# Optimization experiments

Measured on AMD Instinct MI355X. Metric: run time of the kernel, lower is better.

## Reference

```python
import jax, jax.numpy as jnp
import numpy as np


def quantize_ternary(w):
    # BitNet b1.58: scale by mean |w|, round, clamp to {-1,0,1}
    gamma = jnp.maximum(jnp.mean(jnp.abs(w)), 1e-8)
    return jnp.clip(jnp.round(w / gamma), -1.0, 1.0)


def setup_inputs() -> dict:
    key = jax.random.key(0)
    k1, k2, k3 = jax.random.split(key, 3)
    in_features, out_features = 4096, 4096
    x = jax.random.normal(k1, (4, 2048, in_features), dtype=jnp.float32)
    # kaiming_uniform-like init
    bound_w = 1.0 / np.sqrt(in_features)
    weight = jax.random.uniform(k2, (out_features, in_features), dtype=jnp.float32,
                                minval=-bound_w * np.sqrt(3.0), maxval=bound_w * np.sqrt(3.0))
    bias = jax.random.uniform(k3, (out_features,), dtype=jnp.float32,
                              minval=-bound_w, maxval=bound_w)
    return {"x": x, "weight": weight, "bias": bias}


def reference(x, weight, bias):
    qw = quantize_ternary(weight)  # [out, in], values in {-1,0,1}
    # F.linear: x @ qw.T + bias
    return jnp.einsum('bsi,oi->bso', x, qw) + bias
```

## Files before the change

### kernel.cpp

```cpp
#include <hip/hip_runtime.h>
#include <stdint.h>

#define M_DIM 8192
#define N_DIM 4096
#define K_DIM 4096
#define BM 256
#define BN 256
#define BKS 64
#define NSLAB (K_DIM / BKS)
#define SLOT_BYTES (256 * BKS)

typedef int i32x4 __attribute__((ext_vector_type(4)));

__device__ __forceinline__ void async_copy16(const void* g, void* l) {
    __builtin_amdgcn_global_load_lds(
        (const __attribute__((address_space(1))) void*)g,
        (__attribute__((address_space(3))) void*)l, 16, 0, 0);
}

__global__ __launch_bounds__(256) void abssum_partial(const float4* __restrict__ w,
                                                      double* __restrict__ partials) {
    const int lane = threadIdx.x & 63;
    const int wave = threadIdx.x >> 6;
    int base = blockIdx.x * 4096 + threadIdx.x;
    float s = 0.f;
    #pragma unroll
    for (int i = 0; i < 16; i++) {
        float4 v = w[base + i * 256];
        s += fabsf(v.x) + fabsf(v.y) + fabsf(v.z) + fabsf(v.w);
    }
    double d = (double)s;
    #pragma unroll
    for (int off = 32; off > 0; off >>= 1) d += __shfl_down(d, off, 64);
    __shared__ double wsum[4];
    if (lane == 0) wsum[wave] = d;
    __syncthreads();
    if (threadIdx.x == 0)
        partials[blockIdx.x] = (wsum[0] + wsum[1]) + (wsum[2] + wsum[3]);
}

__global__ __launch_bounds__(256) void gamma_reduce(const double* __restrict__ partials,
                                                    float* __restrict__ gamma_out) {
    const int lane = threadIdx.x & 63;
    const int wave = threadIdx.x >> 6;
    double d = partials[threadIdx.x] + partials[threadIdx.x + 256] +
               partials[threadIdx.x + 512] + partials[threadIdx.x + 768];
    #pragma unroll
    for (int off = 32; off > 0; off >>= 1) d += __shfl_down(d, off, 64);
    __shared__ double wsum[4];
    if (lane == 0) wsum[wave] = d;
    __syncthreads();
    if (threadIdx.x == 0) {
        double total = (wsum[0] + wsum[1]) + (wsum[2] + wsum[3]);
        float g = (float)(total * (1.0 / 16777216.0));
        gamma_out[0] = fmaxf(g, 1e-8f);
    }
}

__global__ __launch_bounds__(256) void wquant(const float4* __restrict__ w,
                                              char4* __restrict__ qw,
                                              const float* __restrict__ gamma_p, int n4) {
    float gamma = gamma_p[0];
    int i = blockIdx.x * blockDim.x + threadIdx.x;
    if (i >= n4) return;
    float4 v = w[i];
    char4 o;
    o.x = (signed char)fminf(fmaxf(rintf(v.x / gamma), -1.f), 1.f);
    o.y = (signed char)fminf(fmaxf(rintf(v.y / gamma), -1.f), 1.f);
    o.z = (signed char)fminf(fmaxf(rintf(v.z / gamma), -1.f), 1.f);
    o.w = (signed char)fminf(fmaxf(rintf(v.w / gamma), -1.f), 1.f);
    qw[i] = o;
}

__global__ __launch_bounds__(256) void xquant(const float4* __restrict__ x,
                                              char4* __restrict__ xq,
                                              float* __restrict__ xscale) {
    const int row = blockIdx.x;
    const int lane = threadIdx.x & 63;
    const int wave = threadIdx.x >> 6;
    const float4* xr = x + (size_t)row * (K_DIM / 4);
    float4 v[4];
    float m = 0.f;
    #pragma unroll
    for (int i = 0; i < 4; i++) {
        v[i] = xr[threadIdx.x + i * 256];
        m = fmaxf(m, fmaxf(fmaxf(fabsf(v[i].x), fabsf(v[i].y)),
                           fmaxf(fabsf(v[i].z), fabsf(v[i].w))));
    }
    #pragma unroll
    for (int off = 32; off > 0; off >>= 1) m = fmaxf(m, __shfl_down(m, off, 64));
    __shared__ float wmax[4];
    if (lane == 0) wmax[wave] = m;
    __syncthreads();
    const float mx = fmaxf(fmaxf(wmax[0], wmax[1]), fmaxf(wmax[2], wmax[3]));
    const float scale = fmaxf(mx * (1.f / 127.f), 1e-30f);
    const float inv = 1.f / scale;
    if (threadIdx.x == 0) xscale[row] = scale;
    char4* oq = xq + (size_t)row * (K_DIM / 4);
    #pragma unroll
    for (int i = 0; i < 4; i++) {
        char4 o;
        o.x = (signed char)fminf(fmaxf(rintf(v[i].x * inv), -127.f), 127.f);
        o.y = (signed char)fminf(fmaxf(rintf(v[i].y * inv), -127.f), 127.f);
        o.z = (signed char)fminf(fmaxf(rintf(v[i].z * inv), -127.f), 127.f);
        o.w = (signed char)fminf(fmaxf(rintf(v[i].w * inv), -127.f), 127.f);
        oq[threadIdx.x + i * 256] = o;
    }
}

__global__ __launch_bounds__(512, 2) void gemm_kernel(
    const char* __restrict__ xq,
    const char* __restrict__ qw,
    const float* __restrict__ xscale,
    const float* __restrict__ bias,
    float* __restrict__ out)
{
    __shared__ __align__(16) char As[4][SLOT_BYTES];
    __shared__ __align__(16) char Bs[4][SLOT_BYTES];

    const int tid  = threadIdx.x;
    const int wave = tid >> 6;
    const int lane = tid & 63;
    const int wm   = (wave >> 2) * 128;
    const int wn   = (wave & 3) * 64;
    const int lm   = lane & 15;
    const int q4   = lane >> 4;

    const int bm = blockIdx.y * BM;
    const int bn = blockIdx.x * BN;

    const int rsub = lane >> 2;
    const int csw  = (lane & 3) ^ ((lane >> 3) & 3);
    const char* gA[2];
    const char* gB[2];
    int ldsOff[2];
    #pragma unroll
    for (int j = 0; j < 2; j++) {
        const int r = wave * 32 + j * 16 + rsub;
        gA[j] = xq + (size_t)(bm + r) * K_DIM + csw * 16;
        gB[j] = qw + (size_t)(bn + r) * K_DIM + csw * 16;
        ldsOff[j] = (wave * 32 + j * 16) * BKS;
    }

    i32x4 acc[8][4];
    #pragma unroll
    for (int i = 0; i < 8; i++)
        #pragma unroll
        for (int j = 0; j < 4; j++) acc[i][j] = (i32x4){0, 0, 0, 0};

    const int pc = (q4 ^ ((lm >> 1) & 3)) * 16;

    auto stage_slab = [&](int ts, int slot) {
        async_copy16(gA[0] + (size_t)ts * BKS, &As[slot][ldsOff[0]]);
        async_copy16(gB[0] + (size_t)ts * BKS, &Bs[slot][ldsOff[0]]);
        async_copy16(gA[1] + (size_t)ts * BKS, &As[slot][ldsOff[1]]);
        async_copy16(gB[1] + (size_t)ts * BKS, &Bs[slot][ldsOff[1]]);
    };

    auto compute_slab = [&](const char* Ab, const char* Bb) {
        i32x4 b[4], a[8];
        #pragma unroll
        for (int ni = 0; ni < 4; ni++)
            b[ni] = *(const i32x4*)(Bb + (wn + ni * 16 + lm) * BKS + pc);
        #pragma unroll
        for (int mi = 0; mi < 8; mi++)
            a[mi] = *(const i32x4*)(Ab + (wm + mi * 16 + lm) * BKS + pc);
        __builtin_amdgcn_s_setprio(1);
        #pragma unroll
        for (int mi = 0; mi < 8; mi++)
            #pragma unroll
            for (int ni = 0; ni < 4; ni++)
                acc[mi][ni] = __builtin_amdgcn_mfma_i32_16x16x64_i8(
                    a[mi], b[ni], acc[mi][ni], 0, 0, 0);
        __builtin_amdgcn_s_setprio(0);
    };

    #pragma unroll
    for (int s = 0; s < 3; s++) stage_slab(s, s);
    asm volatile("s_waitcnt vmcnt(8)" ::: "memory");
    __builtin_amdgcn_s_barrier();

    for (int tb = 0; tb < NSLAB - 4; tb += 4) {
        #pragma unroll
        for (int u = 0; u < 4; u++) {
            stage_slab(tb + u + 3, (u + 3) & 3);
            compute_slab(As[u], Bs[u]);
            asm volatile("s_waitcnt vmcnt(8)" ::: "memory");
            __builtin_amdgcn_s_barrier();
        }
    }

    stage_slab(63, 3);
    compute_slab(As[0], Bs[0]);
    asm volatile("s_waitcnt vmcnt(8)" ::: "memory");
    __builtin_amdgcn_s_barrier();

    compute_slab(As[1], Bs[1]);
    asm volatile("s_waitcnt vmcnt(4)" ::: "memory");
    __builtin_amdgcn_s_barrier();

    compute_slab(As[2], Bs[2]);
    asm volatile("s_waitcnt vmcnt(0)" ::: "memory");
    __builtin_amdgcn_s_barrier();

    compute_slab(As[3], Bs[3]);

    float bl[4];
    #pragma unroll
    for (int ni = 0; ni < 4; ni++) bl[ni] = bias[bn + wn + ni * 16 + lm];

    #pragma unroll
    for (int mi = 0; mi < 8; mi++) {
        #pragma unroll
        for (int r = 0; r < 4; r++) {
            const int grow = bm + wm + mi * 16 + q4 * 4 + r;
            const float sc = xscale[grow];
            float* orow = out + (size_t)grow * N_DIM + bn + wn;
            #pragma unroll
            for (int ni = 0; ni < 4; ni++)
                orow[ni * 16 + lm] = sc * (float)acc[mi][ni][r] + bl[ni];
        }
    }
}

extern "C" void kernel_launch(void* const* d_in, const int* in_sizes, int n_in,
                              void* d_out, int out_size, void* d_ws, size_t ws_size,
                              hipStream_t stream) {
    const float* x    = (const float*)d_in[0];
    const float* w    = (const float*)d_in[1];
    const float* bias = (const float*)d_in[2];
    float* out = (float*)d_out;

    char* ws = (char*)d_ws;
    char*   xq       = ws;
    char*   qw       = ws + (size_t)M_DIM * K_DIM;
    float*  xscale   = (float*)(qw + (size_t)N_DIM * K_DIM);
    double* partials = (double*)(xscale + M_DIM);
    float*  gamma_p  = (float*)(partials + 1024);

    const int wn4 = (N_DIM * K_DIM) / 4;

    abssum_partial<<<1024, 256, 0, stream>>>((const float4*)w, partials);
    gamma_reduce<<<1, 256, 0, stream>>>(partials, gamma_p);
    wquant<<<(wn4 + 255) / 256, 256, 0, stream>>>((const float4*)w, (char4*)qw, gamma_p, wn4);
    xquant<<<M_DIM, 256, 0, stream>>>((const float4*)x, (char4*)xq, xscale);

    dim3 grid(N_DIM / BN, M_DIM / BM);
    gemm_kernel<<<grid, 512, 0, stream>>>(xq, qw, xscale, bias, out);
}
```

Before: 413.6 us.

## Fuse quantization prep kernels and shrink GEMM tile to 256x128 with triple buffering

The weight abs-sum and the activation quantization now run in one launch. The gamma reduction is folded into the weight-quantization kernel, which recomputes gamma in every block. Together this cuts four prep launches down to two. The GEMM block goes from 512 threads with a 256x256 tile and 4-slot LDS ring to 256 threads with a 256x128 tile and a 3-slot ring, which lowers LDS use and doubles the number of blocks. The trade-off is more redundant A loads from global memory per output and a shallower prefetch depth.

```diff
diff --git a/kernel.cpp b/kernel.cpp
--- a/kernel.cpp
+++ b/kernel.cpp
@@ -5,10 +5,11 @@
 #define N_DIM 4096
 #define K_DIM 4096
 #define BM 256
-#define BN 256
+#define BN 128
 #define BKS 64
 #define NSLAB (K_DIM / BKS)
-#define SLOT_BYTES (256 * BKS)
+#define A_SLOT (BM * BKS)
+#define B_SLOT (BN * BKS)
 
 typedef int i32x4 __attribute__((ext_vector_type(4)));
 
@@ -18,29 +19,70 @@
         (__attribute__((address_space(3))) void*)l, 16, 0, 0);
 }
 
-__global__ __launch_bounds__(256) void abssum_partial(const float4* __restrict__ w,
-                                                      double* __restrict__ partials) {
+__global__ __launch_bounds__(256) void prep_kernel(
+    const float4* __restrict__ w,
+    const float4* __restrict__ x,
+    double* __restrict__ partials,
+    char4* __restrict__ xq,
+    float* __restrict__ xscale)
+{
     const int lane = threadIdx.x & 63;
     const int wave = threadIdx.x >> 6;
-    int base = blockIdx.x * 4096 + threadIdx.x;
-    float s = 0.f;
-    #pragma unroll
-    for (int i = 0; i < 16; i++) {
-        float4 v = w[base + i * 256];
-        s += fabsf(v.x) + fabsf(v.y) + fabsf(v.z) + fabsf(v.w);
-    }
-    double d = (double)s;
-    #pragma unroll
-    for (int off = 32; off > 0; off >>= 1) d += __shfl_down(d, off, 64);
-    __shared__ double wsum[4];
-    if (lane == 0) wsum[wave] = d;
-    __syncthreads();
-    if (threadIdx.x == 0)
-        partials[blockIdx.x] = (wsum[0] + wsum[1]) + (wsum[2] + wsum[3]);
-}
-
-__global__ __launch_bounds__(256) void gamma_reduce(const double* __restrict__ partials,
-                                                    float* __restrict__ gamma_out) {
+
+    if (blockIdx.x < 1024) {
+        int base = blockIdx.x * 4096 + threadIdx.x;
+        float s = 0.f;
+        #pragma unroll
+        for (int i = 0; i < 16; i++) {
+            float4 v = w[base + i * 256];
+            s += fabsf(v.x) + fabsf(v.y) + fabsf(v.z) + fabsf(v.w);
+        }
+        double d = (double)s;
+        #pragma unroll
+        for (int off = 32; off > 0; off >>= 1) d += __shfl_down(d, off, 64);
+        __shared__ double wsum[4];
+        if (lane == 0) wsum[wave] = d;
+        __syncthreads();
+        if (threadIdx.x == 0)
+            partials[blockIdx.x] = (wsum[0] + wsum[1]) + (wsum[2] + wsum[3]);
+    } else {
+        const int row = blockIdx.x - 1024;
+        const float4* xr = x + (size_t)row * (K_DIM / 4);
+        float4 v[4];
+        float m = 0.f;
+        #pragma unroll
+        for (int i = 0; i < 4; i++) {
+            v[i] = xr[threadIdx.x + i * 256];
+            m = fmaxf(m, fmaxf(fmaxf(fabsf(v[i].x), fabsf(v[i].y)),
+                               fmaxf(fabsf(v[i].z), fabsf(v[i].w))));
+        }
+        #pragma unroll
+        for (int off = 32; off > 0; off >>= 1) m = fmaxf(m, __shfl_down(m, off, 64));
+        __shared__ float wmax[4];
+        if (lane == 0) wmax[wave] = m;
+        __syncthreads();
+        const float mx = fmaxf(fmaxf(wmax[0], wmax[1]), fmaxf(wmax[2], wmax[3]));
+        const float scale = fmaxf(mx * (1.f / 127.f), 1e-30f);
+        const float inv = 1.f / scale;
+        if (threadIdx.x == 0) xscale[row] = scale;
+        char4* oq = xq + (size_t)row * (K_DIM / 4);
+        #pragma unroll
+        for (int i = 0; i < 4; i++) {
+            char4 o;
+            o.x = (signed char)fminf(fmaxf(rintf(v[i].x * inv), -127.f), 127.f);
+            o.y = (signed char)fminf(fmaxf(rintf(v[i].y * inv), -127.f), 127.f);
+            o.z = (signed char)fminf(fmaxf(rintf(v[i].z * inv), -127.f), 127.f);
+            o.w = (signed char)fminf(fmaxf(rintf(v[i].w * inv), -127.f), 127.f);
+            oq[threadIdx.x + i * 256] = o;
+        }
+    }
+}
+
+__global__ __launch_bounds__(256) void wquant_kernel(
+    const double* __restrict__ partials,
+    const float4* __restrict__ w,
+    char4* __restrict__ qw)
+{
     const int lane = threadIdx.x & 63;
     const int wave = threadIdx.x >> 6;
     double d = partials[threadIdx.x] + partials[threadIdx.x + 256] +
@@ -49,80 +91,43 @@
     for (int off = 32; off > 0; off >>= 1) d += __shfl_down(d, off, 64);
     __shared__ double wsum[4];
     if (lane == 0) wsum[wave] = d;
+    __shared__ float gsh;
     __syncthreads();
     if (threadIdx.x == 0) {
         double total = (wsum[0] + wsum[1]) + (wsum[2] + wsum[3]);
-        float g = (float)(total * (1.0 / 16777216.0));
-        gamma_out[0] = fmaxf(g, 1e-8f);
-    }
-}
-
-__global__ __launch_bounds__(256) void wquant(const float4* __restrict__ w,
-                                              char4* __restrict__ qw,
-                                              const float* __restrict__ gamma_p, int n4) {
-    float gamma = gamma_p[0];
-    int i = blockIdx.x * blockDim.x + threadIdx.x;
-    if (i >= n4) return;
-    float4 v = w[i];
-    char4 o;
-    o.x = (signed char)fminf(fmaxf(rintf(v.x / gamma), -1.f), 1.f);
-    o.y = (signed char)fminf(fmaxf(rintf(v.y / gamma), -1.f), 1.f);
-    o.z = (signed char)fminf(fmaxf(rintf(v.z / gamma), -1.f), 1.f);
-    o.w = (signed char)fminf(fmaxf(rintf(v.w / gamma), -1.f), 1.f);
-    qw[i] = o;
-}
-
-__global__ __launch_bounds__(256) void xquant(const float4* __restrict__ x,
-                                              char4* __restrict__ xq,
-                                              float* __restrict__ xscale) {
-    const int row = blockIdx.x;
-    const int lane = threadIdx.x & 63;
-    const int wave = threadIdx.x >> 6;
-    const float4* xr = x + (size_t)row * (K_DIM / 4);
-    float4 v[4];
-    float m = 0.f;
-    #pragma unroll
-    for (int i = 0; i < 4; i++) {
-        v[i] = xr[threadIdx.x + i * 256];
-        m = fmaxf(m, fmaxf(fmaxf(fabsf(v[i].x), fabsf(v[i].y)),
-                           fmaxf(fabsf(v[i].z), fabsf(v[i].w))));
-    }
-    #pragma unroll
-    for (int off = 32; off > 0; off >>= 1) m = fmaxf(m, __shfl_down(m, off, 64));
-    __shared__ float wmax[4];
-    if (lane == 0) wmax[wave] = m;
+        gsh = fmaxf((float)(total * (1.0 / 16777216.0)), 1e-8f);
+    }
     __syncthreads();
-    const float mx = fmaxf(fmaxf(wmax[0], wmax[1]), fmaxf(wmax[2], wmax[3]));
-    const float scale = fmaxf(mx * (1.f / 127.f), 1e-30f);
-    const float inv = 1.f / scale;
-    if (threadIdx.x == 0) xscale[row] = scale;
-    char4* oq = xq + (size_t)row * (K_DIM / 4);
-    #pragma unroll
-    for (int i = 0; i < 4; i++) {
+    const float gamma = gsh;
+
+    int base = blockIdx.x * 4096 + threadIdx.x;
+    #pragma unroll
+    for (int j = 0; j < 16; j++) {
+        float4 v = w[base + j * 256];
         char4 o;
-        o.x = (signed char)fminf(fmaxf(rintf(v[i].x * inv), -127.f), 127.f);
-        o.y = (signed char)fminf(fmaxf(rintf(v[i].y * inv), -127.f), 127.f);
-        o.z = (signed char)fminf(fmaxf(rintf(v[i].z * inv), -127.f), 127.f);
-        o.w = (signed char)fminf(fmaxf(rintf(v[i].w * inv), -127.f), 127.f);
-        oq[threadIdx.x + i * 256] = o;
-    }
-}
-
-__global__ __launch_bounds__(512, 2) void gemm_kernel(
+        o.x = (signed char)fminf(fmaxf(rintf(v.x / gamma), -1.f), 1.f);
+        o.y = (signed char)fminf(fmaxf(rintf(v.y / gamma), -1.f), 1.f);
+        o.z = (signed char)fminf(fmaxf(rintf(v.z / gamma), -1.f), 1.f);
+        o.w = (signed char)fminf(fmaxf(rintf(v.w / gamma), -1.f), 1.f);
+        qw[base + j * 256] = o;
+    }
+}
+
+__global__ __launch_bounds__(256, 2) void gemm_kernel(
     const char* __restrict__ xq,
     const char* __restrict__ qw,
     const float* __restrict__ xscale,
     const float* __restrict__ bias,
     float* __restrict__ out)
 {
-    __shared__ __align__(16) char As[4][SLOT_BYTES];
-    __shared__ __align__(16) char Bs[4][SLOT_BYTES];
+    __shared__ __align__(16) char As[3][A_SLOT];
+    __shared__ __align__(16) char Bs[3][B_SLOT];
 
     const int tid  = threadIdx.x;
     const int wave = tid >> 6;
     const int lane = tid & 63;
-    const int wm   = (wave >> 2) * 128;
-    const int wn   = (wave & 3) * 64;
+    const int wm   = (wave >> 1) * 128;
+    const int wn   = (wave & 1) * 64;
     const int lm   = lane & 15;
     const int q4   = lane >> 4;
 
@@ -131,15 +136,21 @@
 
     const int rsub = lane >> 2;
     const int csw  = (lane & 3) ^ ((lane >> 3) & 3);
-    const char* gA[2];
+    const char* gA[4];
+    int ldsOffA[4];
+    #pragma unroll
+    for (int j = 0; j < 4; j++) {
+        const int r = wave * 64 + j * 16 + rsub;
+        gA[j] = xq + (size_t)(bm + r) * K_DIM + csw * 16;
+        ldsOffA[j] = (wave * 64 + j * 16) * BKS;
+    }
     const char* gB[2];
-    int ldsOff[2];
+    int ldsOffB[2];
     #pragma unroll
     for (int j = 0; j < 2; j++) {
         const int r = wave * 32 + j * 16 + rsub;
-        gA[j] = xq + (size_t)(bm + r) * K_DIM + csw * 16;
         gB[j] = qw + (size_t)(bn + r) * K_DIM + csw * 16;
-        ldsOff[j] = (wave * 32 + j * 16) * BKS;
+        ldsOffB[j] = (wave * 32 + j * 16) * BKS;
     }
 
     i32x4 acc[8][4];
@@ -151,10 +162,12 @@
     const int pc = (q4 ^ ((lm >> 1) & 3)) * 16;
 
     auto stage_slab = [&](int ts, int slot) {
-        async_copy16(gA[0] + (size_t)ts * BKS, &As[slot][ldsOff[0]]);
-        async_copy16(gB[0] + (size_t)ts * BKS, &Bs[slot][ldsOff[0]]);
-        async_copy16(gA[1] + (size_t)ts * BKS, &As[slot][ldsOff[1]]);
-        async_copy16(gB[1] + (size_t)ts * BKS, &Bs[slot][ldsOff[1]]);
+        #pragma unroll
+        for (int j = 0; j < 4; j++)
+            async_copy16(gA[j] + (size_t)ts * BKS, &As[slot][ldsOffA[j]]);
+        #pragma unroll
+        for (int j = 0; j < 2; j++)
+            async_copy16(gB[j] + (size_t)ts * BKS, &Bs[slot][ldsOffB[j]]);
     };
 
     auto compute_slab = [&](const char* Ab, const char* Bb) {
@@ -175,35 +188,36 @@
         __builtin_amdgcn_s_setprio(0);
     };
 
-    #pragma unroll
-    for (int s = 0; s < 3; s++) stage_slab(s, s);
-    asm volatile("s_waitcnt vmcnt(8)" ::: "memory");
-    __builtin_amdgcn_s_barrier();
-
-    for (int tb = 0; tb < NSLAB - 4; tb += 4) {
-        #pragma unroll
-        for (int u = 0; u < 4; u++) {
-            stage_slab(tb + u + 3, (u + 3) & 3);
+    stage_slab(0, 0);
+    stage_slab(1, 1);
+    asm volatile("s_waitcnt vmcnt(6)" ::: "memory");
+    __builtin_amdgcn_s_barrier();
+
+    for (int tb = 0; tb < 60; tb += 3) {
+        #pragma unroll
+        for (int u = 0; u < 3; u++) {
+            stage_slab(tb + u + 2, (u + 2) % 3);
             compute_slab(As[u], Bs[u]);
-            asm volatile("s_waitcnt vmcnt(8)" ::: "memory");
+            asm volatile("s_waitcnt vmcnt(6)" ::: "memory");
             __builtin_amdgcn_s_barrier();
         }
     }
 
-    stage_slab(63, 3);
+    stage_slab(62, 2);
     compute_slab(As[0], Bs[0]);
-    asm volatile("s_waitcnt vmcnt(8)" ::: "memory");
-    __builtin_amdgcn_s_barrier();
-
+    asm volatile("s_waitcnt vmcnt(6)" ::: "memory");
+    __builtin_amdgcn_s_barrier();
+
+    stage_slab(63, 0);
     compute_slab(As[1], Bs[1]);
-    asm volatile("s_waitcnt vmcnt(4)" ::: "memory");
+    asm volatile("s_waitcnt vmcnt(6)" ::: "memory");
     __builtin_amdgcn_s_barrier();
 
     compute_slab(As[2], Bs[2]);
     asm volatile("s_waitcnt vmcnt(0)" ::: "memory");
     __builtin_amdgcn_s_barrier();
 
-    compute_slab(As[3], Bs[3]);
+    compute_slab(As[0], Bs[0]);
 
     float bl[4];
     #pragma unroll
@@ -237,14 +251,12 @@
     float*  xscale   = (float*)(qw + (size_t)N_DIM * K_DIM);
     double* partials = (double*)(xscale + M_DIM);
     float*  gamma_p  = (float*)(partials + 1024);
-
-    const int wn4 = (N_DIM * K_DIM) / 4;
-
-    abssum_partial<<<1024, 256, 0, stream>>>((const float4*)w, partials);
-    gamma_reduce<<<1, 256, 0, stream>>>(partials, gamma_p);
-    wquant<<<(wn4 + 255) / 256, 256, 0, stream>>>((const float4*)w, (char4*)qw, gamma_p, wn4);
-    xquant<<<M_DIM, 256, 0, stream>>>((const float4*)x, (char4*)xq, xscale);
+    (void)gamma_p;
+
+    prep_kernel<<<1024 + M_DIM, 256, 0, stream>>>(
+        (const float4*)w, (const float4*)x, partials, (char4*)xq, xscale);
+    wquant_kernel<<<1024, 256, 0, stream>>>(partials, (const float4*)w, (char4*)qw);
 
     dim3 grid(N_DIM / BN, M_DIM / BM);
-    gemm_kernel<<<grid, 512, 0, stream>>>(xq, qw, xscale, bias, out);
-}
+    gemm_kernel<<<grid, 256, 0, stream>>>(xq, qw, xscale, bias, out);
+}
```

New measurement: 410.5 us. Within noise of the previous version (-0.8%).
